# Kernel tuning notes

Hardware: AMD Instinct MI355X
Metric: run time of the kernel (lower is better)

## Reference

```python
import jax, jax.numpy as jnp
import numpy as np
import math

B, S, H, NH = 2, 2048, 2048, 16
HD = H // NH  # 128
NEG = -1e9


def setup_inputs() -> dict:
    key = jax.random.key(0)
    ks = jax.random.split(key, 6)
    x = jax.random.normal(ks[0], (B, S, H), dtype=jnp.float32)
    # realistic rotary frequencies: cos/sin interleaved, shape [S, HD//2, 2]
    inv_freq = 1.0 / (10000.0 ** (np.arange(0, HD, 2, dtype=np.float32) / HD))
    t = np.arange(S, dtype=np.float32)
    ang = np.outer(t, inv_freq)  # [S, HD//2]
    freqs_cis = jnp.asarray(np.stack([np.cos(ang), np.sin(ang)], axis=-1), dtype=jnp.float32)
    # additive causal mask [1,1,S,S]
    causal = jnp.triu(jnp.full((S, S), NEG, dtype=jnp.float32), k=1)[None, None]
    scale = 0.02
    wq = jax.random.normal(ks[1], (H, H), dtype=jnp.float32) * scale
    wk = jax.random.normal(ks[2], (H, H), dtype=jnp.float32) * scale
    wv = jax.random.normal(ks[3], (H, H), dtype=jnp.float32) * scale
    wo = jax.random.normal(ks[4], (H, H), dtype=jnp.float32) * scale
    position_ids = jnp.broadcast_to(jnp.arange(S, dtype=jnp.int64)[None, :], (B, S))
    return {"x": x, "freqs_cis": freqs_cis, "attention_mask": causal,
            "wq": wq, "wk": wk, "wv": wv, "wo": wo, "position_ids": position_ids}


def _apply_rotary(t, freqs):
    # t: [B,S,NH,HD], freqs: [B,S,1,HD//2,2]
    b, s, nh, hd = t.shape
    tp = t.reshape(b, s, nh, hd // 2, 2)
    tr, ti = tp[..., 0], tp[..., 1]
    fr, fi = freqs[..., 0], freqs[..., 1]
    out = jnp.stack([tr * fr - ti * fi, tr * fi + ti * fr], axis=-1)
    return out.reshape(b, s, nh, hd)


def reference(x, freqs_cis, attention_mask, wq, wk, wv, wo, position_ids):
    b, s, h = x.shape
    q = (x @ wq.T).reshape(b, s, NH, HD)
    k = (x @ wk.T).reshape(b, s, NH, HD)
    v = (x @ wv.T).reshape(b, s, NH, HD)
    freqs = freqs_cis[position_ids][:, :, None]  # [B,S,1,HD//2,2]
    q = _apply_rotary(q, freqs)
    k = _apply_rotary(k, freqs)
    # [B,NH,S,HD]
    q = q.transpose(0, 2, 1, 3)
    k = k.transpose(0, 2, 1, 3)
    v = v.transpose(0, 2, 1, 3)
    scores = jnp.einsum('bhqd,bhkd->bhqk', q, k) / math.sqrt(HD)
    scores = scores + attention_mask
    attn = jax.nn.softmax(scores, axis=-1)
    out = jnp.einsum('bhqk,bhkd->bhqd', attn, v)
    out = out.transpose(0, 2, 1, 3).reshape(b, s, h)
    return out @ wo.T
```

## Files before the change

### kernel.cpp

```cpp
#include <hip/hip_runtime.h>

#define DEVI __device__ __forceinline__

typedef unsigned short u16;
typedef unsigned int   u32;
typedef __attribute__((ext_vector_type(4))) float f32x4;
typedef __attribute__((ext_vector_type(8))) short short8;
typedef __attribute__((ext_vector_type(8))) __bf16 bf16x8;

#define B_   2
#define S_   2048
#define H_   2048
#define NH_  16
#define HD_  128
#define BH_  (B_*NH_)
#define QSCALE 0.12751743f

DEVI u16 f2b(float f){
  u32 u = __builtin_bit_cast(u32, f);
  u32 r = (u + 0x7fffu + ((u >> 16) & 1u)) >> 16;
  return (u16)r;
}
DEVI float b2f(u16 h){
  u32 u = ((u32)h) << 16;
  return __builtin_bit_cast(float, u);
}
DEVI u32 cvt_pk_bf16(float lo, float hi){
  u32 r; asm("v_cvt_pk_bf16_f32 %0, %1, %2" : "=v"(r) : "v"(lo), "v"(hi)); return r;
}
DEVI u32 rot2(u16 lo, u16 hi, float c, float s, float scale){
  float tr = b2f(lo), ti = b2f(hi);
  return cvt_pk_bf16((tr*c - ti*s)*scale, (tr*s + ti*c)*scale);
}
DEVI f32x4 mfma_bf16(short8 a, short8 b, f32x4 c){
  return __builtin_amdgcn_mfma_f32_16x16x32_bf16(
      __builtin_bit_cast(bf16x8, a), __builtin_bit_cast(bf16x8, b), c, 0, 0, 0);
}
DEVI void gl_lds16(const void* g, void* l){
  __builtin_amdgcn_global_load_lds((const __attribute__((address_space(1))) void*)g,
                                   (__attribute__((address_space(3))) void*)l, 16, 0, 0);
}

template<int LOG2CPR>
DEVI void stage_swz(const u16* __restrict__ src, int srcStride , u16* lds, int tid){
  const int wid = tid >> 6, lane = tid & 63;
#pragma unroll
  for (int i = 0; i < 4; ++i){
    int lin = i*256 + wid*64 + lane;
    int row = lin >> LOG2CPR;
    int cb  = ((lin & ((1 << LOG2CPR) - 1)) * 16) ^ ((row & 7) << 4);
    gl_lds16(src + (size_t)row * srcStride + (cb >> 1),
             lds + (size_t)(i*256 + wid*64) * 8);
  }
}

__global__ __launch_bounds__(256) void cvt5_kernel(
    const float* __restrict__ x,  const float* __restrict__ wq,
    const float* __restrict__ wk, const float* __restrict__ wv,
    const float* __restrict__ wo, u16* __restrict__ xb,
    u16* __restrict__ wqkv, u16* __restrict__ wob){
  int i = blockIdx.x * 256 + threadIdx.x;
  const float* src; u16* dst; int off;
  if      (i < 2097152){ src = x;  dst = xb;             off = i;           }
  else if (i < 3145728){ src = wq; dst = wqkv;           off = i - 2097152; }
  else if (i < 4194304){ src = wk; dst = wqkv + 4194304; off = i - 3145728; }
  else if (i < 5242880){ src = wv; dst = wqkv + 8388608; off = i - 4194304; }
  else                 { src = wo; dst = wob;            off = i - 5242880; }
  float4 v = ((const float4*)src)[off];
  uint2 o;
  o.x = (u32)f2b(v.x) | ((u32)f2b(v.y) << 16);
  o.y = (u32)f2b(v.z) | ((u32)f2b(v.w) << 16);
  ((uint2*)dst)[off] = o;
}

template<int EPI>
__global__ __launch_bounds__(256) void gemm_bt(
    const u16* __restrict__ A, const u16* __restrict__ Bw,
    float* __restrict__ C, u16* __restrict__ Qd, u16* __restrict__ Kd, u16* __restrict__ Vd,
    int M, int N, int K)
{
  __shared__ __align__(16) u16 As[128*64];
  __shared__ __align__(16) u16 Bs[128*64];
  const int tid  = threadIdx.x, lane = tid & 63, wid = tid >> 6;
  const int wr   = wid >> 1, wc = wid & 1;
  const int lrow = lane & 15, lk = lane >> 4;
  const int RB = blockIdx.y * 128, CB = blockIdx.x * 128;
  f32x4 acc[4][4] = {};

  for (int k0 = 0; k0 < K; k0 += 64){
    __syncthreads();
    stage_swz<3>(A  + (size_t)RB * K + k0, K, As, tid);
    stage_swz<3>(Bw + (size_t)CB * K + k0, K, Bs, tid);
    __syncthreads();
#pragma unroll
    for (int kk = 0; kk < 2; ++kk){
      short8 af[4], bf[4];
#pragma unroll
      for (int m = 0; m < 4; ++m){
        int row = wr*64 + m*16 + lrow;
        int cb  = (kk*64 + lk*16) ^ ((row & 7) << 4);
        af[m] = *(const short8*)&As[row*64 + (cb >> 1)];
      }
#pragma unroll
      for (int n = 0; n < 4; ++n){
        int row = wc*64 + n*16 + lrow;
        int cb  = (kk*64 + lk*16) ^ ((row & 7) << 4);
        bf[n] = *(const short8*)&Bs[row*64 + (cb >> 1)];
      }
#pragma unroll
      for (int m = 0; m < 4; ++m)
#pragma unroll
        for (int n = 0; n < 4; ++n)
          acc[m][n] = mfma_bf16(af[m], bf[n], acc[m][n]);
    }
  }

#pragma unroll
  for (int m = 0; m < 4; ++m){
#pragma unroll
    for (int n = 0; n < 4; ++n){
#pragma unroll
      for (int r = 0; r < 4; ++r){
        int row = RB + wr*64 + m*16 + lk*4 + r;
        int col = CB + wc*64 + n*16 + lrow;
        float v = acc[m][n][r];
        if constexpr (EPI == 0){
          C[(size_t)row * N + col] = v;
        } else {
          int which = col >> 11;
          int hd = col & 2047;
          int h = hd >> 7, d = hd & 127;
          int b = row >> 11, s = row & 2047;
          u16* dst = (which == 0) ? Qd : (which == 1) ? Kd : Vd;
          dst[(((size_t)(b*NH_ + h)) * S_ + s) * HD_ + d] = f2b(v);
        }
      }
    }
  }
}

__global__ __launch_bounds__(256) void rope_k_kernel(u16* __restrict__ K,
                                                     const float* __restrict__ F){
  int idx = blockIdx.x * 256 + threadIdx.x;
  int d2 = idx & 63;
  int s  = (idx >> 6) & (S_ - 1);
  int bh = idx >> 17;
  size_t off = ((size_t)bh * S_ + s) * HD_ + d2*2;
  float c = F[s*128 + d2*2], sn = F[s*128 + d2*2 + 1];
  u32 kp = *(const u32*)(K + off);
  float tr = b2f((u16)kp), ti = b2f((u16)(kp >> 16));
  *(u32*)(K + off) = (u32)f2b(tr*c - ti*sn) | ((u32)f2b(tr*sn + ti*c) << 16);
}

__global__ void transpose_v(const u16* __restrict__ V, u16* __restrict__ Vt){
  __shared__ u16 t[32][33];
  int s0 = blockIdx.x * 32, d0 = blockIdx.y * 32, bh = blockIdx.z;
  const u16* vb = V  + (size_t)bh * S_ * HD_;
  u16*       tb = Vt + (size_t)bh * HD_ * S_;
  int tx = threadIdx.x, ty = threadIdx.y;
#pragma unroll
  for (int i = 0; i < 4; ++i)
    t[ty + i*8][tx] = vb[(size_t)(s0 + ty + i*8) * HD_ + d0 + tx];
  __syncthreads();
#pragma unroll
  for (int i = 0; i < 4; ++i)
    tb[(size_t)(d0 + ty + i*8) * S_ + s0 + tx] = t[tx][ty + i*8];
}

__global__ __launch_bounds__(256) void attn_kernel(
    const u16* __restrict__ Q, const u16* __restrict__ K, const u16* __restrict__ Vt,
    const float* __restrict__ F, u16* __restrict__ O)
{
  __shared__ __align__(16) u16 Ks[2][64*128];
  __shared__ __align__(16) u16 Vs[2][128*64];
  __shared__ __align__(16) u16 Ps[4][16*64];
  const int tid  = threadIdx.x, lane = tid & 63, wid = tid >> 6;
  const int lrow = lane & 15, lk = lane >> 4;

  const int lin = blockIdx.x;
  const int bh  = (lin & 7) | ((lin >> 7) << 3);
  const int x   = (lin >> 3) & 15;

  const u16* Kb  = K  + (size_t)bh * S_ * HD_;
  const u16* Vtb = Vt + (size_t)bh * HD_ * S_;
  const int b = bh >> 4, h = bh & 15;
  u16* const pw = &Ps[wid][0];

  for (int pass = 0; pass < 2; ++pass){
    const int qb = pass ? x : (31 - x);
    const int q0 = qb * 64;
    const int ntile = qb + 1;
    const int qg = q0 + wid*16 + lrow;

    short8 qf[4];
    {
      const u16* qp_ = Q + ((size_t)bh * S_ + qg) * HD_;
      const float* Fq = F + (size_t)qg * 128;
#pragma unroll
      for (int kc = 0; kc < 4; ++kc){
        short8 q = *(const short8*)&qp_[kc*32 + lk*8];
        float4 fa = *(const float4*)&Fq[kc*32 + lk*8];
        float4 fb = *(const float4*)&Fq[kc*32 + lk*8 + 4];
        uint4 w;
        w.x = rot2((u16)q[0], (u16)q[1], fa.x, fa.y, QSCALE);
        w.y = rot2((u16)q[2], (u16)q[3], fa.z, fa.w, QSCALE);
        w.z = rot2((u16)q[4], (u16)q[5], fb.x, fb.y, QSCALE);
        w.w = rot2((u16)q[6], (u16)q[7], fb.z, fb.w, QSCALE);
        qf[kc] = __builtin_bit_cast(short8, w);
      }
    }

    f32x4 acco[8] = {};
    float m_ = -3.0e38f, l_ = 0.0f;

    int cur = 0;
    stage_swz<4>(Kb,  HD_, &Ks[0][0], tid);
    stage_swz<3>(Vtb, S_,  &Vs[0][0], tid);
    __syncthreads();

    for (int t = 0; t < ntile; ++t){
      if (t + 1 < ntile){
        stage_swz<4>(Kb  + (size_t)(t+1)*64*HD_, HD_, &Ks[cur^1][0], tid);
        stage_swz<3>(Vtb + (t+1)*64,             S_,  &Vs[cur^1][0], tid);
      }
      const int kv0 = t*64;
      const u16* ks = &Ks[cur][0];
      const u16* vs = &Vs[cur][0];

      f32x4 sc[4] = {};
      __builtin_amdgcn_s_setprio(1);
#pragma unroll
      for (int nt = 0; nt < 4; ++nt){
        int row = nt*16 + lrow;
#pragma unroll
        for (int kc = 0; kc < 4; ++kc){
          int cb = (kc*64 + lk*16) ^ ((row & 7) << 4);
          short8 kf = *(const short8*)&ks[row*128 + (cb >> 1)];
          sc[nt] = mfma_bf16(kf, qf[kc], sc[nt]);
        }
      }
      __builtin_amdgcn_s_setprio(0);

      if (t == ntile - 1){
#pragma unroll
        for (int nt = 0; nt < 4; ++nt)
#pragma unroll
          for (int r = 0; r < 4; ++r)
            if (kv0 + nt*16 + lk*4 + r > qg) sc[nt][r] = -1.0e30f;
      }

      {
        float pmax = sc[0][0];
#pragma unroll
        for (int nt = 0; nt < 4; ++nt)
#pragma unroll
          for (int r = 0; r < 4; ++r) pmax = fmaxf(pmax, sc[nt][r]);
        pmax = fmaxf(pmax, __shfl_xor(pmax, 16));
        pmax = fmaxf(pmax, __shfl_xor(pmax, 32));
        if (!__all(pmax - m_ <= 11.0f)){
          float mn = fmaxf(m_, pmax);
          float c = exp2f(m_ - mn);
          l_ *= c;
#pragma unroll
          for (int dt = 0; dt < 8; ++dt)
#pragma unroll
            for (int r = 0; r < 4; ++r) acco[dt][r] *= c;
          m_ = mn;
        }
        float rs = 0.0f;
#pragma unroll
        for (int nt = 0; nt < 4; ++nt)
#pragma unroll
          for (int r = 0; r < 4; ++r){
            float p = exp2f(sc[nt][r] - m_);
            sc[nt][r] = p;
            rs += p;
          }
        rs += __shfl_xor(rs, 16);
        rs += __shfl_xor(rs, 32);
        l_ += rs;
#pragma unroll
        for (int nt = 0; nt < 4; ++nt){
          uint2 wv;
          wv.x = cvt_pk_bf16(sc[nt][0], sc[nt][1]);
          wv.y = cvt_pk_bf16(sc[nt][2], sc[nt][3]);
          int boff = (nt*32 + lk*8) ^ ((lrow & 7) << 4);
          *(uint2*)((char*)&pw[lrow*64] + boff) = wv;
        }
      }

#pragma unroll
      for (int kc2 = 0; kc2 < 2; ++kc2){
        int pboff = (kc2*64 + lk*16) ^ ((lrow & 7) << 4);
        short8 pf = *(const short8*)((const char*)&pw[lrow*64] + pboff);
        __builtin_amdgcn_s_setprio(1);
#pragma unroll
        for (int dt = 0; dt < 8; ++dt){
          int row = dt*16 + lrow;
          int cb = (kc2*64 + lk*16) ^ ((row & 7) << 4);
          short8 vf = *(const short8*)&vs[row*64 + (cb >> 1)];
          acco[dt] = mfma_bf16(vf, pf, acco[dt]);
        }
        __builtin_amdgcn_s_setprio(0);
      }

      __syncthreads();
      cur ^= 1;
    }

    {
      float inv = 1.0f / l_;
      u16* ob = O + ((size_t)(b*S_ + qg)) * H_ + h*128;
#pragma unroll
      for (int dt = 0; dt < 8; ++dt){
        uint2 wv;
        wv.x = cvt_pk_bf16(acco[dt][0]*inv, acco[dt][1]*inv);
        wv.y = cvt_pk_bf16(acco[dt][2]*inv, acco[dt][3]*inv);
        *(uint2*)&ob[dt*16 + lk*4] = wv;
      }
    }
    __syncthreads();
  }
}

extern "C" void kernel_launch(void* const* d_in, const int* in_sizes, int n_in,
                              void* d_out, int out_size, void* d_ws, size_t ws_size,
                              hipStream_t stream)
{
  (void)in_sizes; (void)n_in; (void)out_size; (void)ws_size;
  const float* x  = (const float*)d_in[0];
  const float* fc = (const float*)d_in[1];
  const float* wq = (const float*)d_in[3];
  const float* wk = (const float*)d_in[4];
  const float* wv = (const float*)d_in[5];
  const float* wo = (const float*)d_in[6];

  char* w = (char*)d_ws;
  u16* xb   = (u16*)(w);
  u16* wqkv = (u16*)(w + 16777216);
  u16* wob  = (u16*)(w + 41943040);
  u16* Qr   = (u16*)(w + 50331648);
  u16* Kr   = (u16*)(w + 67108864);
  u16* Vr   = (u16*)(w + 83886080);
  u16* Vt   = (u16*)(w + 100663296);
  u16* aO   = (u16*)(w + 117440512);
  float* out = (float*)d_out;

  cvt5_kernel<<<24576, 256, 0, stream>>>(x, wq, wk, wv, wo, xb, wqkv, wob);

  gemm_bt<1><<<dim3(48, 32), 256, 0, stream>>>(xb, wqkv, nullptr, Qr, Kr, Vr, 4096, 6144, 2048);
  rope_k_kernel<<<16384, 256, 0, stream>>>(Kr, fc);
  transpose_v<<<dim3(64, 4, 32), dim3(32, 8), 0, stream>>>(Vr, Vt);
  attn_kernel<<<512, 256, 0, stream>>>(Qr, Kr, Vt, fc, aO);
  gemm_bt<0><<<dim3(16, 32), 256, 0, stream>>>(aO, wob, out, nullptr, nullptr, nullptr, 4096, 2048, 2048);
}
```

Baseline: 276.2 us.

## Replace QKV GEMM with 256x128 triple-buffered 8-wave pipelined kernel

Adds a new QKV projection GEMM that uses 512 threads, 256x128 output tiles and three LDS stages of 64-wide K slices. Global-to-LDS loads for stage t+2 are spread across the four compute phases of each iteration, and the MFMA sections run at raised wave priority. A block-index swizzle groups tiles for L2 locality. The aim is to hide load latency and raise MFMA utilization, at the cost of 144KB dynamic LDS per block (one block per CU) and more barriers.

```diff
diff --git a/kernel.cpp b/kernel.cpp
--- a/kernel.cpp
+++ b/kernel.cpp
@@ -51,6 +51,17 @@
     int cb  = ((lin & ((1 << LOG2CPR) - 1)) * 16) ^ ((row & 7) << 4);
     gl_lds16(src + (size_t)row * srcStride + (cb >> 1),
              lds + (size_t)(i*256 + wid*64) * 8);
+  }
+}
+
+DEVI void stage2(const u16* __restrict__ src, u16* lds, int tid, int it0){
+#pragma unroll
+  for (int i = it0; i < it0 + 2; ++i){
+    int lin = i*512 + tid;
+    int row = lin >> 3;
+    int cb  = ((lin & 7) * 16) ^ ((row & 7) << 4);
+    gl_lds16(src + (size_t)row * 2048 + (cb >> 1),
+             lds + (size_t)(i*512 + (tid & ~63)) * 8);
   }
 }
 
@@ -73,6 +84,97 @@
   ((uint2*)dst)[off] = o;
 }
 
+#define G8_NT 32
+__global__ __launch_bounds__(512) void gemm8_qkv(
+    const u16* __restrict__ A, const u16* __restrict__ Bw,
+    u16* __restrict__ Qd, u16* __restrict__ Kd, u16* __restrict__ Vd)
+{
+  extern __shared__ __align__(16) u16 lds[];
+  const int tid = threadIdx.x, lane = tid & 63, wid = tid >> 6;
+  const int wm = wid >> 2, wn = wid & 3;
+  const int lrow = lane & 15, lk = lane >> 4;
+  const int swzb = (blockIdx.x & 7) * 96 + (blockIdx.x >> 3);
+  const int RB = (swzb / 48) * 256, CB = (swzb % 48) * 128;
+  const u16* Ab = A  + (size_t)RB * 2048;
+  const u16* Bb = Bw + (size_t)CB * 2048;
+
+  f32x4 acc[8][2] = {};
+
+#define AS_(s) (lds + (s) * 24576)
+#define BS_(s) (lds + (s) * 24576 + 16384)
+
+  stage2(Ab,      AS_(0), tid, 0);  stage2(Ab,      AS_(0), tid, 2);
+  stage2(Bb,      BS_(0), tid, 0);
+  stage2(Ab + 64, AS_(1), tid, 0);  stage2(Ab + 64, AS_(1), tid, 2);
+  stage2(Bb + 64, BS_(1), tid, 0);
+  asm volatile("s_waitcnt vmcnt(6)" ::: "memory");
+  __builtin_amdgcn_s_barrier();
+
+  for (int t = 0; t < G8_NT; ++t){
+    const u16* as = AS_(t % 3);
+    const u16* bs = BS_(t % 3);
+    const int  ns = (t + 2) % 3;
+    const bool st = (t + 2 < G8_NT);
+    const u16* an = Ab + (t + 2) * 64;
+    const u16* bn = Bb + (t + 2) * 64;
+
+#pragma unroll
+    for (int ph = 0; ph < 4; ++ph){
+      const int mh = ph & 1, kh = ph >> 1;
+      short8 af[4], bf[2];
+#pragma unroll
+      for (int i = 0; i < 4; ++i){
+        int row = wm*128 + (mh*4 + i)*16 + lrow;
+        int cb  = (kh*64 + lk*16) ^ ((row & 7) << 4);
+        af[i] = *(const short8*)&as[row*64 + (cb >> 1)];
+      }
+#pragma unroll
+      for (int j = 0; j < 2; ++j){
+        int row = wn*32 + j*16 + lrow;
+        int cb  = (kh*64 + lk*16) ^ ((row & 7) << 4);
+        bf[j] = *(const short8*)&bs[row*64 + (cb >> 1)];
+      }
+      if (st){
+        if      (ph == 0) stage2(an, AS_(ns), tid, 0);
+        else if (ph == 1) stage2(an, AS_(ns), tid, 2);
+        else if (ph == 2) stage2(bn, BS_(ns), tid, 0);
+      }
+      __builtin_amdgcn_s_barrier();
+      __builtin_amdgcn_s_setprio(1);
+#pragma unroll
+      for (int i = 0; i < 4; ++i)
+#pragma unroll
+        for (int j = 0; j < 2; ++j)
+          acc[mh*4 + i][j] = mfma_bf16(af[i], bf[j], acc[mh*4 + i][j]);
+      __builtin_amdgcn_s_setprio(0);
+      if (ph < 3) __builtin_amdgcn_s_barrier();
+    }
+    if (st)                   asm volatile("s_waitcnt vmcnt(6)" ::: "memory");
+    else if (t + 1 < G8_NT)   asm volatile("s_waitcnt vmcnt(0)" ::: "memory");
+    __builtin_amdgcn_s_barrier();
+  }
+
+#pragma unroll
+  for (int fm = 0; fm < 8; ++fm){
+#pragma unroll
+    for (int fn = 0; fn < 2; ++fn){
+      const int col  = CB + wn*32 + fn*16 + lrow;
+      const int row0 = RB + wm*128 + fm*16 + lk*4;
+      const int which = col >> 11;
+      const int hd = col & 2047;
+      const int h = hd >> 7, d = hd & 127;
+      const int b = row0 >> 11, s0 = row0 & 2047;
+      u16* dst = (which == 0) ? Qd : (which == 1) ? Kd : Vd;
+      size_t base = (((size_t)(b*NH_ + h)) * S_ + s0) * HD_ + d;
+#pragma unroll
+      for (int r = 0; r < 4; ++r)
+        dst[base + (size_t)r * HD_] = f2b(acc[fm][fn][r]);
+    }
+  }
+#undef AS_
+#undef BS_
+}
+
 template<int EPI>
 __global__ __launch_bounds__(256) void gemm_bt(
     const u16* __restrict__ A, const u16* __restrict__ Bw,
@@ -346,9 +448,12 @@
   u16* aO   = (u16*)(w + 117440512);
   float* out = (float*)d_out;
 
+  (void)hipFuncSetAttribute((const void*)gemm8_qkv,
+                            hipFuncAttributeMaxDynamicSharedMemorySize, 147456);
+
   cvt5_kernel<<<24576, 256, 0, stream>>>(x, wq, wk, wv, wo, xb, wqkv, wob);
 
-  gemm_bt<1><<<dim3(48, 32), 256, 0, stream>>>(xb, wqkv, nullptr, Qr, Kr, Vr, 4096, 6144, 2048);
+  gemm8_qkv<<<768, 512, 147456, stream>>>(xb, wqkv, Qr, Kr, Vr);
   rope_k_kernel<<<16384, 256, 0, stream>>>(Kr, fc);
   transpose_v<<<dim3(64, 4, 32), dim3(32, 8), 0, stream>>>(Vr, Vt);
   attn_kernel<<<512, 256, 0, stream>>>(Qr, Kr, Vt, fc, aO);
```

Measured after the change: 275.2 us. No clear change (-0.4%).
